# Optimization experiments

Measured on AMD Instinct MI355X. Metric: run time of the kernel, lower is better.

Reference implementation:

```python
import jax, jax.numpy as jnp
import numpy as np

B, N, D, K, S = 16, 1024, 256, 16, 512
TEMP = 0.5   # self.temperature, set externally in the repo
EPS = 1e-10


def _gumbel(key, shape):
    u = jax.random.uniform(key, shape, dtype=jnp.float32)
    return -jnp.log(-jnp.log(u + EPS) + EPS)


def setup_inputs() -> dict:
    key = jax.random.key(0)
    k1, k2, k3 = jax.random.split(key, 3)
    return {
        "ze": jax.random.normal(k1, (B, N, D), dtype=jnp.float32),
        "c_logits": jax.random.normal(k2, (B, K), dtype=jnp.float32),
        "books": jax.random.normal(k3, (K, S, D), dtype=jnp.float32),
        "log_param_q": jnp.asarray(np.log(0.5), dtype=jnp.float32),
        "log_param_q_cls": jnp.asarray(np.log(0.5), dtype=jnp.float32),
        "is_train": 1,
    }


def reference(ze, c_logits, books, log_param_q, log_param_q_cls, is_train):
    # training-path forward of GaussianVectorQuantizer
    param_q = 1.0 + jnp.exp(log_param_q)
    precision_q = 0.5 / jnp.clip(param_q, 1e-10)
    param_q_cls = 1.0 + jnp.exp(log_param_q_cls)
    precision_q_cls = 0.5 / jnp.clip(param_q_cls, 1e-10)

    gkey = jax.random.key(42)
    kg1, kg2 = jax.random.split(gkey)

    # gumbel-softmax over clusters: (B, K)
    c_probs = jax.nn.softmax(
        (c_logits * precision_q_cls + _gumbel(kg1, c_logits.shape)) / TEMP, axis=-1
    )

    # pairwise squared distances to every codebook entry of every cluster: (B, N, K, S)
    z2 = jnp.sum(ze * ze, axis=-1)[:, :, None, None]          # (B, N, 1, 1)
    b2 = jnp.sum(books * books, axis=-1)[None, None]          # (1, 1, K, S)
    cross = jnp.einsum('bnd,ksd->bnks', ze, books)            # (B, N, K, S)
    logit_all = -(z2 - 2.0 * cross + b2) * precision_q        # (B, N, K, S)

    # cluster-probability-weighted logits: (B, N, S)
    logits = jnp.einsum('bnks,bk->bns', logit_all, c_probs)

    # gumbel-softmax encodings per cluster, then weighted codebook matmul
    enc = jax.nn.softmax((logit_all + _gumbel(kg2, logit_all.shape)) / TEMP, axis=-1)
    zq = jnp.einsum('bnks,ksd,bk->bnd', enc, books, c_probs)  # (B, N, D)

    prob = jax.nn.softmax(logits, axis=-1)
    log_prob = jax.nn.log_softmax(logits, axis=-1)
    return zq, precision_q, prob, log_prob
```

## Files before the change

kernel.cpp:

```cpp
#include <hip/hip_runtime.h>
#include <cstdint>
#include <cstddef>

#define JAX_PARTITIONABLE 1

namespace {

constexpr int Bsz = 16, Nn = 1024, Dd = 256, Kk = 16, Ss = 512;
constexpr uint32_t BN = (uint32_t)Bsz * Nn;
constexpr int ZQ_SIZE = Bsz * Nn * Dd;
constexpr int PQ_OFF = ZQ_SIZE;
constexpr int PROB_OFF = ZQ_SIZE + 1;
constexpr int BNS = Bsz * Nn * Ss;
constexpr int LP_OFF = PROB_OFF + BNS;

constexpr int WS_CP = 0;
constexpr int WS_B2 = 256;
constexpr int WS_WB2 = WS_B2 + Kk * Ss;
constexpr int WS_WBF = WS_WB2 + Bsz * Ss;
constexpr int WS_BBF = WS_WBF + Bsz * Ss * Dd;
constexpr int WS_BTF = WS_BBF + (Kk * Ss * Dd) / 2;

constexpr float LOG2E = 1.4426950408889634f;

typedef __attribute__((ext_vector_type(8))) short bf16x8;
typedef __attribute__((ext_vector_type(4))) short short4v;
typedef __attribute__((ext_vector_type(4))) float f32x4;

__device__ __forceinline__ float hw_exp2(float x) { return __builtin_amdgcn_exp2f(x); }
__device__ __forceinline__ float hw_log2(float x) { return __builtin_amdgcn_logf(x); }

struct KP { uint32_t a, b; };

__host__ __device__ constexpr KP tf2x32(uint32_t k0, uint32_t k1,
                                        uint32_t x0, uint32_t x1) {
  uint32_t ks[3] = {k0, k1, k0 ^ k1 ^ 0x1BD11BDAu};
  const int rot[2][4] = {{13, 15, 26, 6}, {17, 29, 16, 24}};
  x0 += ks[0];
  x1 += ks[1];
#pragma unroll
  for (int i = 0; i < 5; ++i) {
#pragma unroll
    for (int j = 0; j < 4; ++j) {
      int r = rot[i & 1][j];
      x0 += x1;
      x1 = (x1 << r) | (x1 >> (32 - r));
      x1 ^= x0;
    }
    x0 += ks[(i + 1) % 3];
    x1 += ks[(i + 2) % 3] + (uint32_t)(i + 1);
  }
  return {x0, x1};
}

#if JAX_PARTITIONABLE
constexpr KP KG1 = tf2x32(0u, 42u, 0u, 0u);
constexpr KP KG2 = tf2x32(0u, 42u, 0u, 1u);
#else
constexpr KP KH0 = tf2x32(0u, 42u, 0u, 2u);
constexpr KP KH1 = tf2x32(0u, 42u, 1u, 3u);
constexpr KP KG1 = {KH0.a, KH1.a};
constexpr KP KG2 = {KH0.b, KH1.b};
#endif

__device__ __forceinline__ float jax_gumbel(KP key, uint32_t idx, uint32_t half) {
#if JAX_PARTITIONABLE
  (void)half;
  KP h = tf2x32(key.a, key.b, 0u, idx);
  uint32_t bits = h.a ^ h.b;
#else
  uint32_t lo = idx < half ? idx : idx - half;
  KP h = tf2x32(key.a, key.b, lo, lo + half);
  uint32_t bits = idx < half ? h.a : h.b;
#endif
  float u = __uint_as_float((bits >> 9) | 0x3F800000u) - 1.0f;
  return -__logf(-__logf(u + 1e-10f) + 1e-10f);
}

__device__ __forceinline__ float jax_gumbel_w2(KP key, uint32_t idx) {
  KP h = tf2x32(key.a, key.b, 0u, idx);
  uint32_t bits = h.a ^ h.b;
  float u = __uint_as_float((bits >> 9) | 0x3F800000u) - 1.0f;
  float y = -__logf(u + 1e-10f) + 1e-10f;
  return -2.0f * hw_log2(y);
}

__device__ __forceinline__ float prec_q(const float* p) {
  return 0.5f / fmaxf(1.0f + expf(p[0]), 1e-10f);
}

__device__ __forceinline__ short f2bf(float x) {
  uint32_t u = __float_as_uint(x);
  uint32_t r = (u + 0x7FFFu + ((u >> 16) & 1u)) >> 16;
  return (short)r;
}

__global__ void __launch_bounds__(256) cprobs_kernel(
    const float* __restrict__ c_logits, const float* __restrict__ lpq,
    const float* __restrict__ lpq_cls, float* __restrict__ ws,
    float* __restrict__ out) {
  __shared__ float sl[256];
  const int t = threadIdx.x;
  const float pqc = prec_q(lpq_cls);
  float g = jax_gumbel(KG1, (uint32_t)t, 128u);
  sl[t] = (c_logits[t] * pqc + g) * 2.0f;
  __syncthreads();
  const int b = t >> 4;
  float m = -3.0e38f;
  for (int j = 0; j < 16; ++j) m = fmaxf(m, sl[b * 16 + j]);
  float sum = 0.f;
  for (int j = 0; j < 16; ++j) sum += expf(sl[b * 16 + j] - m);
  ws[WS_CP + t] = expf(sl[t] - m) / sum;
  if (t == 0) out[PQ_OFF] = prec_q(lpq);
}

__global__ void __launch_bounds__(256) norms_kernel(
    const float* __restrict__ books, float* __restrict__ ws) {
  const int row = blockIdx.x * 4 + (threadIdx.x >> 6);
  const int lane = threadIdx.x & 63;
  float4 v = ((const float4*)(books + (size_t)row * Dd))[lane];
  float s = v.x * v.x + v.y * v.y + v.z * v.z + v.w * v.w;
#pragma unroll
  for (int d = 1; d < 64; d <<= 1) s += __shfl_xor(s, d);
  if (lane == 0) ws[WS_B2 + row] = s;
}

__global__ void __launch_bounds__(256) prep_kernel(
    const float* __restrict__ books, float* __restrict__ ws) {
  __shared__ short tile[16 * 256];
  const int k = blockIdx.x >> 5;
  const int s0 = (blockIdx.x & 31) << 4;
  short* bbf = (short*)(ws + WS_BBF);
  short* btf = (short*)(ws + WS_BTF);
  const int t = threadIdx.x;
#pragma unroll
  for (int i = 0; i < 4; ++i) {
    int idx = t + 256 * i;
    int r = idx >> 6, dq = idx & 63;
    float4 v = ((const float4*)books)[(size_t)(k * Ss + s0 + r) * 64 + dq];
    short4v h = {f2bf(v.x), f2bf(v.y), f2bf(v.z), f2bf(v.w)};
    *(short4v*)&bbf[(size_t)(k * Ss + s0 + r) * 256 + dq * 4] = h;
    *(short4v*)&tile[r * 256 + dq * 4] = h;
  }
  __syncthreads();
  const int d = t;
  short vals[16];
#pragma unroll
  for (int r = 0; r < 16; ++r) vals[r] = tile[r * 256 + d];
  bf16x8 lo, hi;
#pragma unroll
  for (int r = 0; r < 8; ++r) { lo[r] = vals[r]; hi[r] = vals[r + 8]; }
  size_t base = ((size_t)(k * 256 + d)) * 512 + s0;
  *(bf16x8*)&btf[base] = lo;
  *(bf16x8*)&btf[base + 8] = hi;
}

__global__ void __launch_bounds__(256) wbooks_kernel(
    const float* __restrict__ books, float* __restrict__ ws) {
  const int bs = blockIdx.x;
  const int b = bs >> 9, s = bs & 511;
  const int d = threadIdx.x;
  const float* cp = ws + WS_CP + b * 16;
  float acc = 0.f;
#pragma unroll
  for (int k = 0; k < 16; ++k)
    acc = fmaf(cp[k], books[((size_t)(k * Ss + s)) * Dd + d], acc);
  short* wbf = (short*)(ws + WS_WBF);
  wbf[((size_t)(b * Ss + s)) * Dd + d] = f2bf(acc);
  if (d == 0) {
    float a2 = 0.f;
#pragma unroll
    for (int k = 0; k < 16; ++k) a2 = fmaf(cp[k], ws[WS_B2 + k * Ss + s], a2);
    ws[WS_WB2 + b * Ss + s] = a2;
  }
}

__global__ void __launch_bounds__(512, 4) fused_kernel(
    const float* __restrict__ ze, const float* __restrict__ lpq,
    const float* __restrict__ ws, float* __restrict__ out) {
  __shared__ short ze_s[32 * 264];
  __shared__ short enc_s[32 * 520];
  __shared__ float2 redms[32][9];
  __shared__ float cpk[16];

  const int t = threadIdx.x;
  const int w = t >> 6, lane = t & 63, c = lane & 15, q = lane >> 4;
  const float pq = prec_q(lpq);

  if (blockIdx.x < 512) {
    const int b = blockIdx.x >> 5;
    const int n0 = (blockIdx.x & 31) << 5;
    const short* bbf = (const short*)(ws + WS_BBF);
    const short* btf = (const short*)(ws + WS_BTF);
    const float* b2p = ws + WS_B2;
    const float ca = 4.f * pq * LOG2E;
    const float cbs = -2.f * pq * LOG2E;

    if (t < 16) cpk[t] = ws[WS_CP + b * 16 + t];
#pragma unroll
    for (int i = 0; i < 4; ++i) {
      int idx = t + 512 * i;
      int r = idx >> 6, dq = idx & 63;
      float4 v = ((const float4*)ze)[(size_t)(b * Nn + n0 + r) * 64 + dq];
      short4v h = {f2bf(v.x), f2bf(v.y), f2bf(v.z), f2bf(v.w)};
      *(short4v*)&ze_s[r * 264 + dq * 4] = h;
    }
    __syncthreads();

    f32x4 acc2[2][2];
#pragma unroll
    for (int rt = 0; rt < 2; ++rt)
#pragma unroll
      for (int dt = 0; dt < 2; ++dt) acc2[rt][dt] = (f32x4)(0.f);

    for (int k = 0; k < 16; ++k) {
      f32x4 acc1[2][4];
#pragma unroll
      for (int rt = 0; rt < 2; ++rt)
#pragma unroll
        for (int st = 0; st < 4; ++st) acc1[rt][st] = (f32x4)(0.f);
      for (int dstep = 0; dstep < 8; ++dstep) {
        bf16x8 a0 = *(const bf16x8*)&ze_s[(c) * 264 + dstep * 32 + q * 8];
        bf16x8 a1 = *(const bf16x8*)&ze_s[(16 + c) * 264 + dstep * 32 + q * 8];
#pragma unroll
        for (int st = 0; st < 4; ++st) {
          bf16x8 bB = *(const bf16x8*)&bbf[((size_t)(k * Ss + w * 64 + st * 16 + c)) * 256 +
                                           dstep * 32 + q * 8];
          acc1[0][st] = __builtin_amdgcn_mfma_f32_16x16x32_bf16(a0, bB, acc1[0][st], 0, 0, 0);
          acc1[1][st] = __builtin_amdgcn_mfma_f32_16x16x32_bf16(a1, bB, acc1[1][st], 0, 0, 0);
        }
      }

      float cb[4];
#pragma unroll
      for (int st = 0; st < 4; ++st) cb[st] = cbs * b2p[k * Ss + w * 64 + st * 16 + c];
      float mx[2][4], sm[2][4];
#pragma unroll
      for (int rt = 0; rt < 2; ++rt)
#pragma unroll
        for (int reg = 0; reg < 4; ++reg) mx[rt][reg] = -3.0e38f;
#pragma unroll
      for (int rt = 0; rt < 2; ++rt)
#pragma unroll
        for (int st = 0; st < 4; ++st)
#pragma unroll
          for (int reg = 0; reg < 4; ++reg) {
            int row = n0 + rt * 16 + q * 4 + reg;
            uint32_t gi = ((uint32_t)(b * Nn + row) * (uint32_t)Kk + (uint32_t)k) * (uint32_t)Ss +
                          (uint32_t)(w * 64 + st * 16 + c);
            float gw = jax_gumbel_w2(KG2, gi);
            float v = fmaf(acc1[rt][st][reg], ca, cb[st]) + gw;
            acc1[rt][st][reg] = v;
            mx[rt][reg] = fmaxf(mx[rt][reg], v);
          }
#pragma unroll
      for (int m = 1; m < 16; m <<= 1)
#pragma unroll
        for (int rt = 0; rt < 2; ++rt)
#pragma unroll
          for (int reg = 0; reg < 4; ++reg)
            mx[rt][reg] = fmaxf(mx[rt][reg], __shfl_xor(mx[rt][reg], m));
#pragma unroll
      for (int rt = 0; rt < 2; ++rt)
#pragma unroll
        for (int reg = 0; reg < 4; ++reg) sm[rt][reg] = 0.f;
#pragma unroll
      for (int rt = 0; rt < 2; ++rt)
#pragma unroll
        for (int st = 0; st < 4; ++st)
#pragma unroll
          for (int reg = 0; reg < 4; ++reg) {
            float e = hw_exp2(acc1[rt][st][reg] - mx[rt][reg]);
            acc1[rt][st][reg] = e;
            sm[rt][reg] += e;
          }
#pragma unroll
      for (int m = 1; m < 16; m <<= 1)
#pragma unroll
        for (int rt = 0; rt < 2; ++rt)
#pragma unroll
          for (int reg = 0; reg < 4; ++reg) sm[rt][reg] += __shfl_xor(sm[rt][reg], m);
      if (c == 0) {
#pragma unroll
        for (int rt = 0; rt < 2; ++rt)
#pragma unroll
          for (int reg = 0; reg < 4; ++reg) {
            int rl = rt * 16 + q * 4 + reg;
            redms[rl][w] = make_float2(mx[rt][reg], sm[rt][reg]);
          }
      }
      __syncthreads();

      const float cpv = cpk[k];
#pragma unroll
      for (int rt = 0; rt < 2; ++rt)
#pragma unroll
        for (int reg = 0; reg < 4; ++reg) {
          int rl = rt * 16 + q * 4 + reg;
          float M = mx[rt][reg];
#pragma unroll
          for (int w2 = 0; w2 < 8; ++w2) M = fmaxf(M, redms[rl][w2].x);
          float T = 0.f;
#pragma unroll
          for (int w2 = 0; w2 < 8; ++w2)
            T = fmaf(redms[rl][w2].y, hw_exp2(redms[rl][w2].x - M), T);
          float scale = cpv * hw_exp2(mx[rt][reg] - M) * __builtin_amdgcn_rcpf(T);
#pragma unroll
          for (int st = 0; st < 4; ++st)
            enc_s[rl * 520 + w * 64 + st * 16 + c] = f2bf(acc1[rt][st][reg] * scale);
        }
      __syncthreads();

      for (int ss = 0; ss < 16; ++ss) {
        bf16x8 a0 = *(const bf16x8*)&enc_s[(c) * 520 + ss * 32 + q * 8];
        bf16x8 a1 = *(const bf16x8*)&enc_s[(16 + c) * 520 + ss * 32 + q * 8];
#pragma unroll
        for (int dt = 0; dt < 2; ++dt) {
          bf16x8 bB = *(const bf16x8*)&btf[((size_t)(k * 256 + w * 32 + dt * 16 + c)) * 512 +
                                           ss * 32 + q * 8];
          acc2[0][dt] = __builtin_amdgcn_mfma_f32_16x16x32_bf16(a0, bB, acc2[0][dt], 0, 0, 0);
          acc2[1][dt] = __builtin_amdgcn_mfma_f32_16x16x32_bf16(a1, bB, acc2[1][dt], 0, 0, 0);
        }
      }
    }

#pragma unroll
    for (int rt = 0; rt < 2; ++rt)
#pragma unroll
      for (int dt = 0; dt < 2; ++dt)
#pragma unroll
        for (int reg = 0; reg < 4; ++reg) {
          int row = n0 + rt * 16 + q * 4 + reg;
          int d = w * 32 + dt * 16 + c;
          out[(size_t)(b * Nn + row) * Dd + d] = acc2[rt][dt][reg];
        }
  } else {
    const int mbid = blockIdx.x - 512;
    const int b = mbid >> 5;
    const int n0 = (mbid & 31) << 5;
    const short* wbf = (const short*)(ws + WS_WBF);
    const float* wb2 = ws + WS_WB2;

#pragma unroll
    for (int i = 0; i < 4; ++i) {
      int idx = t + 512 * i;
      int r = idx >> 6, dq = idx & 63;
      float4 v = ((const float4*)ze)[(size_t)(b * Nn + n0 + r) * 64 + dq];
      short4v h = {f2bf(v.x), f2bf(v.y), f2bf(v.z), f2bf(v.w)};
      *(short4v*)&ze_s[r * 264 + dq * 4] = h;
    }
    __syncthreads();

    f32x4 acc1[2][4];
#pragma unroll
    for (int rt = 0; rt < 2; ++rt)
#pragma unroll
      for (int st = 0; st < 4; ++st) acc1[rt][st] = (f32x4)(0.f);
    for (int dstep = 0; dstep < 8; ++dstep) {
      bf16x8 a0 = *(const bf16x8*)&ze_s[(c) * 264 + dstep * 32 + q * 8];
      bf16x8 a1 = *(const bf16x8*)&ze_s[(16 + c) * 264 + dstep * 32 + q * 8];
#pragma unroll
      for (int st = 0; st < 4; ++st) {
        bf16x8 bB = *(const bf16x8*)&wbf[((size_t)(b * Ss + w * 64 + st * 16 + c)) * 256 +
                                         dstep * 32 + q * 8];
        acc1[0][st] = __builtin_amdgcn_mfma_f32_16x16x32_bf16(a0, bB, acc1[0][st], 0, 0, 0);
        acc1[1][st] = __builtin_amdgcn_mfma_f32_16x16x32_bf16(a1, bB, acc1[1][st], 0, 0, 0);
      }
    }

    float mx[2][4], sm[2][4];
#pragma unroll
    for (int rt = 0; rt < 2; ++rt)
#pragma unroll
      for (int reg = 0; reg < 4; ++reg) mx[rt][reg] = -3.0e38f;
#pragma unroll
    for (int st = 0; st < 4; ++st) {
      const float wb2v = wb2[b * Ss + w * 64 + st * 16 + c];
#pragma unroll
      for (int rt = 0; rt < 2; ++rt)
#pragma unroll
        for (int reg = 0; reg < 4; ++reg) {
          float v = (2.f * acc1[rt][st][reg] - wb2v) * pq;
          acc1[rt][st][reg] = v;
          mx[rt][reg] = fmaxf(mx[rt][reg], v);
        }
    }
#pragma unroll
    for (int m = 1; m < 16; m <<= 1)
#pragma unroll
      for (int rt = 0; rt < 2; ++rt)
#pragma unroll
        for (int reg = 0; reg < 4; ++reg)
          mx[rt][reg] = fmaxf(mx[rt][reg], __shfl_xor(mx[rt][reg], m));
#pragma unroll
    for (int rt = 0; rt < 2; ++rt)
#pragma unroll
      for (int reg = 0; reg < 4; ++reg) sm[rt][reg] = 0.f;
#pragma unroll
    for (int st = 0; st < 4; ++st)
#pragma unroll
      for (int rt = 0; rt < 2; ++rt)
#pragma unroll
        for (int reg = 0; reg < 4; ++reg)
          sm[rt][reg] += __expf(acc1[rt][st][reg] - mx[rt][reg]);
#pragma unroll
    for (int m = 1; m < 16; m <<= 1)
#pragma unroll
      for (int rt = 0; rt < 2; ++rt)
#pragma unroll
        for (int reg = 0; reg < 4; ++reg) sm[rt][reg] += __shfl_xor(sm[rt][reg], m);
    if (c == 0) {
#pragma unroll
      for (int rt = 0; rt < 2; ++rt)
#pragma unroll
        for (int reg = 0; reg < 4; ++reg)
          redms[rt * 16 + q * 4 + reg][w] = make_float2(mx[rt][reg], sm[rt][reg]);
    }
    __syncthreads();

#pragma unroll
    for (int rt = 0; rt < 2; ++rt)
#pragma unroll
      for (int reg = 0; reg < 4; ++reg) {
        int rl = rt * 16 + q * 4 + reg;
        float M = mx[rt][reg];
#pragma unroll
        for (int w2 = 0; w2 < 8; ++w2) M = fmaxf(M, redms[rl][w2].x);
        float T = 0.f;
#pragma unroll
        for (int w2 = 0; w2 < 8; ++w2)
          T = fmaf(redms[rl][w2].y, __expf(redms[rl][w2].x - M), T);
        const float invT = __builtin_amdgcn_rcpf(T);
        const float lT = __logf(T);
        const size_t base = (size_t)(b * Nn + n0 + rl) * Ss;
#pragma unroll
        for (int st = 0; st < 4; ++st) {
          int s = w * 64 + st * 16 + c;
          float v = acc1[rt][st][reg] - M;
          out[PROB_OFF + base + s] = __expf(v) * invT;
          out[LP_OFF + base + s] = v - lT;
        }
      }
  }
}

}

extern "C" void kernel_launch(void* const* d_in, const int* in_sizes, int n_in,
                              void* d_out, int out_size, void* d_ws, size_t ws_size,
                              hipStream_t stream) {
  (void)in_sizes; (void)n_in; (void)out_size; (void)ws_size;
  const float* ze = (const float*)d_in[0];
  const float* c_logits = (const float*)d_in[1];
  const float* books = (const float*)d_in[2];
  const float* lpq = (const float*)d_in[3];
  const float* lpq_cls = (const float*)d_in[4];
  float* out = (float*)d_out;
  float* ws = (float*)d_ws;

  hipLaunchKernelGGL(cprobs_kernel, dim3(1), dim3(256), 0, stream,
                     c_logits, lpq, lpq_cls, ws, out);
  hipLaunchKernelGGL(norms_kernel, dim3(Kk * Ss / 4), dim3(256), 0, stream, books, ws);
  hipLaunchKernelGGL(prep_kernel, dim3(Kk * 32), dim3(256), 0, stream, books, ws);
  hipLaunchKernelGGL(wbooks_kernel, dim3(Bsz * Ss), dim3(256), 0, stream, books, ws);
  hipLaunchKernelGGL(fused_kernel, dim3(1024), dim3(512), 0, stream,
                     ze, lpq, ws, out);
}
```

Measured before the change: 724.0 us.

## Enlarge fused kernel tile to 64 rows with 16 waves per block

The fused kernel now uses 1024-thread blocks that each handle 64 rows instead of 32. Each wave covers 32 codebook columns and 16 output dims across 4 row tiles. The goal is to halve redundant global reads of the bf16 codebooks per row and raise MFMA reuse of each B fragment. The cross-wave softmax reduction becomes a two-step one: 64 threads compute the final max and inverse sum into shared memory, which adds a barrier. The larger block means more LDS per block and fewer blocks (512) in flight, and __launch_bounds__(1024,4) may force register spills.

```diff
diff --git a/kernel.cpp b/kernel.cpp
--- a/kernel.cpp
+++ b/kernel.cpp
@@ -175,21 +175,26 @@
   }
 }
 
-__global__ void __launch_bounds__(512, 4) fused_kernel(
+__global__ void __launch_bounds__(1024, 4) fused_kernel(
     const float* __restrict__ ze, const float* __restrict__ lpq,
     const float* __restrict__ ws, float* __restrict__ out) {
-  __shared__ short ze_s[32 * 264];
-  __shared__ short enc_s[32 * 520];
-  __shared__ float2 redms[32][9];
+  __shared__ short ze_s[64 * 264];
+  __shared__ short enc_s[64 * 520];
+  __shared__ float redmax[64][17];
+  __shared__ float redsum[64][17];
+  __shared__ float finalM[64];
+  __shared__ float finalI[64];
+  __shared__ float finalL[64];
   __shared__ float cpk[16];
 
   const int t = threadIdx.x;
-  const int w = t >> 6, lane = t & 63, c = lane & 15, q = lane >> 4;
+  const int w = t >> 6;
+  const int lane = t & 63, c = lane & 15, q = lane >> 4;
   const float pq = prec_q(lpq);
 
-  if (blockIdx.x < 512) {
-    const int b = blockIdx.x >> 5;
-    const int n0 = (blockIdx.x & 31) << 5;
+  if (blockIdx.x < 256) {
+    const int b = blockIdx.x >> 4;
+    const int n0 = (blockIdx.x & 15) << 6;
     const short* bbf = (const short*)(ws + WS_BBF);
     const short* btf = (const short*)(ws + WS_BTF);
     const float* b2p = ws + WS_B2;
@@ -199,7 +204,7 @@
     if (t < 16) cpk[t] = ws[WS_CP + b * 16 + t];
 #pragma unroll
     for (int i = 0; i < 4; ++i) {
-      int idx = t + 512 * i;
+      int idx = t + 1024 * i;
       int r = idx >> 6, dq = idx & 63;
       float4 v = ((const float4*)ze)[(size_t)(b * Nn + n0 + r) * 64 + dq];
       short4v h = {f2bf(v.x), f2bf(v.y), f2bf(v.z), f2bf(v.w)};
@@ -207,47 +212,48 @@
     }
     __syncthreads();
 
-    f32x4 acc2[2][2];
-#pragma unroll
-    for (int rt = 0; rt < 2; ++rt)
-#pragma unroll
-      for (int dt = 0; dt < 2; ++dt) acc2[rt][dt] = (f32x4)(0.f);
+    f32x4 acc2[4];
+#pragma unroll
+    for (int rt = 0; rt < 4; ++rt) acc2[rt] = (f32x4)(0.f);
 
     for (int k = 0; k < 16; ++k) {
-      f32x4 acc1[2][4];
-#pragma unroll
-      for (int rt = 0; rt < 2; ++rt)
-#pragma unroll
-        for (int st = 0; st < 4; ++st) acc1[rt][st] = (f32x4)(0.f);
+      f32x4 acc1[4][2];
+#pragma unroll
+      for (int rt = 0; rt < 4; ++rt)
+#pragma unroll
+        for (int st = 0; st < 2; ++st) acc1[rt][st] = (f32x4)(0.f);
       for (int dstep = 0; dstep < 8; ++dstep) {
-        bf16x8 a0 = *(const bf16x8*)&ze_s[(c) * 264 + dstep * 32 + q * 8];
-        bf16x8 a1 = *(const bf16x8*)&ze_s[(16 + c) * 264 + dstep * 32 + q * 8];
-#pragma unroll
-        for (int st = 0; st < 4; ++st) {
-          bf16x8 bB = *(const bf16x8*)&bbf[((size_t)(k * Ss + w * 64 + st * 16 + c)) * 256 +
+        bf16x8 a[4];
+#pragma unroll
+        for (int rt = 0; rt < 4; ++rt)
+          a[rt] = *(const bf16x8*)&ze_s[(rt * 16 + c) * 264 + dstep * 32 + q * 8];
+#pragma unroll
+        for (int st = 0; st < 2; ++st) {
+          bf16x8 bB = *(const bf16x8*)&bbf[((size_t)(k * Ss + w * 32 + st * 16 + c)) * 256 +
                                            dstep * 32 + q * 8];
-          acc1[0][st] = __builtin_amdgcn_mfma_f32_16x16x32_bf16(a0, bB, acc1[0][st], 0, 0, 0);
-          acc1[1][st] = __builtin_amdgcn_mfma_f32_16x16x32_bf16(a1, bB, acc1[1][st], 0, 0, 0);
+#pragma unroll
+          for (int rt = 0; rt < 4; ++rt)
+            acc1[rt][st] = __builtin_amdgcn_mfma_f32_16x16x32_bf16(a[rt], bB, acc1[rt][st], 0, 0, 0);
         }
       }
 
-      float cb[4];
-#pragma unroll
-      for (int st = 0; st < 4; ++st) cb[st] = cbs * b2p[k * Ss + w * 64 + st * 16 + c];
-      float mx[2][4], sm[2][4];
-#pragma unroll
-      for (int rt = 0; rt < 2; ++rt)
+      float cb[2];
+#pragma unroll
+      for (int st = 0; st < 2; ++st) cb[st] = cbs * b2p[k * Ss + w * 32 + st * 16 + c];
+      float mx[4][4], sm[4][4];
+#pragma unroll
+      for (int rt = 0; rt < 4; ++rt)
 #pragma unroll
         for (int reg = 0; reg < 4; ++reg) mx[rt][reg] = -3.0e38f;
 #pragma unroll
-      for (int rt = 0; rt < 2; ++rt)
-#pragma unroll
-        for (int st = 0; st < 4; ++st)
+      for (int rt = 0; rt < 4; ++rt)
+#pragma unroll
+        for (int st = 0; st < 2; ++st)
 #pragma unroll
           for (int reg = 0; reg < 4; ++reg) {
             int row = n0 + rt * 16 + q * 4 + reg;
             uint32_t gi = ((uint32_t)(b * Nn + row) * (uint32_t)Kk + (uint32_t)k) * (uint32_t)Ss +
-                          (uint32_t)(w * 64 + st * 16 + c);
+                          (uint32_t)(w * 32 + st * 16 + c);
             float gw = jax_gumbel_w2(KG2, gi);
             float v = fmaf(acc1[rt][st][reg], ca, cb[st]) + gw;
             acc1[rt][st][reg] = v;
@@ -256,94 +262,100 @@
 #pragma unroll
       for (int m = 1; m < 16; m <<= 1)
 #pragma unroll
-        for (int rt = 0; rt < 2; ++rt)
+        for (int rt = 0; rt < 4; ++rt)
 #pragma unroll
           for (int reg = 0; reg < 4; ++reg)
             mx[rt][reg] = fmaxf(mx[rt][reg], __shfl_xor(mx[rt][reg], m));
-#pragma unroll
-      for (int rt = 0; rt < 2; ++rt)
-#pragma unroll
-        for (int reg = 0; reg < 4; ++reg) sm[rt][reg] = 0.f;
-#pragma unroll
-      for (int rt = 0; rt < 2; ++rt)
-#pragma unroll
-        for (int st = 0; st < 4; ++st)
+      float smv[4][4];
+#pragma unroll
+      for (int rt = 0; rt < 4; ++rt)
+#pragma unroll
+        for (int reg = 0; reg < 4; ++reg) smv[rt][reg] = 0.f;
+#pragma unroll
+      for (int rt = 0; rt < 4; ++rt)
+#pragma unroll
+        for (int st = 0; st < 2; ++st)
 #pragma unroll
           for (int reg = 0; reg < 4; ++reg) {
             float e = hw_exp2(acc1[rt][st][reg] - mx[rt][reg]);
             acc1[rt][st][reg] = e;
-            sm[rt][reg] += e;
+            smv[rt][reg] += e;
           }
 #pragma unroll
       for (int m = 1; m < 16; m <<= 1)
 #pragma unroll
-        for (int rt = 0; rt < 2; ++rt)
-#pragma unroll
-          for (int reg = 0; reg < 4; ++reg) sm[rt][reg] += __shfl_xor(sm[rt][reg], m);
+        for (int rt = 0; rt < 4; ++rt)
+#pragma unroll
+          for (int reg = 0; reg < 4; ++reg) smv[rt][reg] += __shfl_xor(smv[rt][reg], m);
       if (c == 0) {
 #pragma unroll
-        for (int rt = 0; rt < 2; ++rt)
+        for (int rt = 0; rt < 4; ++rt)
 #pragma unroll
           for (int reg = 0; reg < 4; ++reg) {
             int rl = rt * 16 + q * 4 + reg;
-            redms[rl][w] = make_float2(mx[rt][reg], sm[rt][reg]);
+            redmax[rl][w] = mx[rt][reg];
+            redsum[rl][w] = smv[rt][reg];
           }
       }
       __syncthreads();
 
+      if (t < 64) {
+        float M = redmax[t][0];
+#pragma unroll
+        for (int w2 = 1; w2 < 16; ++w2) M = fmaxf(M, redmax[t][w2]);
+        float T = 0.f;
+#pragma unroll
+        for (int w2 = 0; w2 < 16; ++w2)
+          T = fmaf(redsum[t][w2], hw_exp2(redmax[t][w2] - M), T);
+        finalM[t] = M;
+        finalI[t] = __builtin_amdgcn_rcpf(T);
+      }
+      __syncthreads();
+
       const float cpv = cpk[k];
 #pragma unroll
-      for (int rt = 0; rt < 2; ++rt)
+      for (int rt = 0; rt < 4; ++rt)
 #pragma unroll
         for (int reg = 0; reg < 4; ++reg) {
           int rl = rt * 16 + q * 4 + reg;
-          float M = mx[rt][reg];
-#pragma unroll
-          for (int w2 = 0; w2 < 8; ++w2) M = fmaxf(M, redms[rl][w2].x);
-          float T = 0.f;
-#pragma unroll
-          for (int w2 = 0; w2 < 8; ++w2)
-            T = fmaf(redms[rl][w2].y, hw_exp2(redms[rl][w2].x - M), T);
-          float scale = cpv * hw_exp2(mx[rt][reg] - M) * __builtin_amdgcn_rcpf(T);
-#pragma unroll
-          for (int st = 0; st < 4; ++st)
-            enc_s[rl * 520 + w * 64 + st * 16 + c] = f2bf(acc1[rt][st][reg] * scale);
+          float scale = cpv * hw_exp2(mx[rt][reg] - finalM[rl]) * finalI[rl];
+#pragma unroll
+          for (int st = 0; st < 2; ++st)
+            enc_s[rl * 520 + w * 32 + st * 16 + c] = f2bf(acc1[rt][st][reg] * scale);
         }
       __syncthreads();
 
       for (int ss = 0; ss < 16; ++ss) {
-        bf16x8 a0 = *(const bf16x8*)&enc_s[(c) * 520 + ss * 32 + q * 8];
-        bf16x8 a1 = *(const bf16x8*)&enc_s[(16 + c) * 520 + ss * 32 + q * 8];
-#pragma unroll
-        for (int dt = 0; dt < 2; ++dt) {
-          bf16x8 bB = *(const bf16x8*)&btf[((size_t)(k * 256 + w * 32 + dt * 16 + c)) * 512 +
-                                           ss * 32 + q * 8];
-          acc2[0][dt] = __builtin_amdgcn_mfma_f32_16x16x32_bf16(a0, bB, acc2[0][dt], 0, 0, 0);
-          acc2[1][dt] = __builtin_amdgcn_mfma_f32_16x16x32_bf16(a1, bB, acc2[1][dt], 0, 0, 0);
-        }
-      }
-    }
-
-#pragma unroll
-    for (int rt = 0; rt < 2; ++rt)
-#pragma unroll
-      for (int dt = 0; dt < 2; ++dt)
-#pragma unroll
-        for (int reg = 0; reg < 4; ++reg) {
-          int row = n0 + rt * 16 + q * 4 + reg;
-          int d = w * 32 + dt * 16 + c;
-          out[(size_t)(b * Nn + row) * Dd + d] = acc2[rt][dt][reg];
-        }
+        bf16x8 a[4];
+#pragma unroll
+        for (int rt = 0; rt < 4; ++rt)
+          a[rt] = *(const bf16x8*)&enc_s[(rt * 16 + c) * 520 + ss * 32 + q * 8];
+        bf16x8 bB = *(const bf16x8*)&btf[((size_t)(k * 256 + w * 16 + c)) * 512 +
+                                         ss * 32 + q * 8];
+#pragma unroll
+        for (int rt = 0; rt < 4; ++rt)
+          acc2[rt] = __builtin_amdgcn_mfma_f32_16x16x32_bf16(a[rt], bB, acc2[rt], 0, 0, 0);
+      }
+    }
+
+#pragma unroll
+    for (int rt = 0; rt < 4; ++rt)
+#pragma unroll
+      for (int reg = 0; reg < 4; ++reg) {
+        int row = n0 + rt * 16 + q * 4 + reg;
+        int d = w * 16 + c;
+        out[(size_t)(b * Nn + row) * Dd + d] = acc2[rt][reg];
+      }
   } else {
-    const int mbid = blockIdx.x - 512;
-    const int b = mbid >> 5;
-    const int n0 = (mbid & 31) << 5;
+    const int mbid = blockIdx.x - 256;
+    const int b = mbid >> 4;
+    const int n0 = (mbid & 15) << 6;
     const short* wbf = (const short*)(ws + WS_WBF);
     const float* wb2 = ws + WS_WB2;
 
 #pragma unroll
     for (int i = 0; i < 4; ++i) {
-      int idx = t + 512 * i;
+      int idx = t + 1024 * i;
       int r = idx >> 6, dq = idx & 63;
       float4 v = ((const float4*)ze)[(size_t)(b * Nn + n0 + r) * 64 + dq];
       short4v h = {f2bf(v.x), f2bf(v.y), f2bf(v.z), f2bf(v.w)};
@@ -351,33 +363,36 @@
     }
     __syncthreads();
 
-    f32x4 acc1[2][4];
-#pragma unroll
-    for (int rt = 0; rt < 2; ++rt)
-#pragma unroll
-      for (int st = 0; st < 4; ++st) acc1[rt][st] = (f32x4)(0.f);
+    f32x4 acc1[4][2];
+#pragma unroll
+    for (int rt = 0; rt < 4; ++rt)
+#pragma unroll
+      for (int st = 0; st < 2; ++st) acc1[rt][st] = (f32x4)(0.f);
     for (int dstep = 0; dstep < 8; ++dstep) {
-      bf16x8 a0 = *(const bf16x8*)&ze_s[(c) * 264 + dstep * 32 + q * 8];
-      bf16x8 a1 = *(const bf16x8*)&ze_s[(16 + c) * 264 + dstep * 32 + q * 8];
-#pragma unroll
-      for (int st = 0; st < 4; ++st) {
-        bf16x8 bB = *(const bf16x8*)&wbf[((size_t)(b * Ss + w * 64 + st * 16 + c)) * 256 +
+      bf16x8 a[4];
+#pragma unroll
+      for (int rt = 0; rt < 4; ++rt)
+        a[rt] = *(const bf16x8*)&ze_s[(rt * 16 + c) * 264 + dstep * 32 + q * 8];
+#pragma unroll
+      for (int st = 0; st < 2; ++st) {
+        bf16x8 bB = *(const bf16x8*)&wbf[((size_t)(b * Ss + w * 32 + st * 16 + c)) * 256 +
                                          dstep * 32 + q * 8];
-        acc1[0][st] = __builtin_amdgcn_mfma_f32_16x16x32_bf16(a0, bB, acc1[0][st], 0, 0, 0);
-        acc1[1][st] = __builtin_amdgcn_mfma_f32_16x16x32_bf16(a1, bB, acc1[1][st], 0, 0, 0);
-      }
-    }
-
-    float mx[2][4], sm[2][4];
-#pragma unroll
-    for (int rt = 0; rt < 2; ++rt)
+#pragma unroll
+        for (int rt = 0; rt < 4; ++rt)
+          acc1[rt][st] = __builtin_amdgcn_mfma_f32_16x16x32_bf16(a[rt], bB, acc1[rt][st], 0, 0, 0);
+      }
+    }
+
+    float mx[4][4], sm[4][4];
+#pragma unroll
+    for (int rt = 0; rt < 4; ++rt)
 #pragma unroll
       for (int reg = 0; reg < 4; ++reg) mx[rt][reg] = -3.0e38f;
 #pragma unroll
-    for (int st = 0; st < 4; ++st) {
-      const float wb2v = wb2[b * Ss + w * 64 + st * 16 + c];
-#pragma unroll
-      for (int rt = 0; rt < 2; ++rt)
+    for (int st = 0; st < 2; ++st) {
+      const float wb2v = wb2[b * Ss + w * 32 + st * 16 + c];
+#pragma unroll
+      for (int rt = 0; rt < 4; ++rt)
 #pragma unroll
         for (int reg = 0; reg < 4; ++reg) {
           float v = (2.f * acc1[rt][st][reg] - wb2v) * pq;
@@ -388,54 +403,65 @@
 #pragma unroll
     for (int m = 1; m < 16; m <<= 1)
 #pragma unroll
-      for (int rt = 0; rt < 2; ++rt)
+      for (int rt = 0; rt < 4; ++rt)
 #pragma unroll
         for (int reg = 0; reg < 4; ++reg)
           mx[rt][reg] = fmaxf(mx[rt][reg], __shfl_xor(mx[rt][reg], m));
 #pragma unroll
-    for (int rt = 0; rt < 2; ++rt)
+    for (int rt = 0; rt < 4; ++rt)
 #pragma unroll
       for (int reg = 0; reg < 4; ++reg) sm[rt][reg] = 0.f;
 #pragma unroll
-    for (int st = 0; st < 4; ++st)
-#pragma unroll
-      for (int rt = 0; rt < 2; ++rt)
+    for (int st = 0; st < 2; ++st)
+#pragma unroll
+      for (int rt = 0; rt < 4; ++rt)
 #pragma unroll
         for (int reg = 0; reg < 4; ++reg)
           sm[rt][reg] += __expf(acc1[rt][st][reg] - mx[rt][reg]);
 #pragma unroll
     for (int m = 1; m < 16; m <<= 1)
 #pragma unroll
-      for (int rt = 0; rt < 2; ++rt)
+      for (int rt = 0; rt < 4; ++rt)
 #pragma unroll
         for (int reg = 0; reg < 4; ++reg) sm[rt][reg] += __shfl_xor(sm[rt][reg], m);
     if (c == 0) {
 #pragma unroll
-      for (int rt = 0; rt < 2; ++rt)
-#pragma unroll
-        for (int reg = 0; reg < 4; ++reg)
-          redms[rt * 16 + q * 4 + reg][w] = make_float2(mx[rt][reg], sm[rt][reg]);
+      for (int rt = 0; rt < 4; ++rt)
+#pragma unroll
+        for (int reg = 0; reg < 4; ++reg) {
+          int rl = rt * 16 + q * 4 + reg;
+          redmax[rl][w] = mx[rt][reg];
+          redsum[rl][w] = sm[rt][reg];
+        }
     }
     __syncthreads();
 
-#pragma unroll
-    for (int rt = 0; rt < 2; ++rt)
+    if (t < 64) {
+      float M = redmax[t][0];
+#pragma unroll
+      for (int w2 = 1; w2 < 16; ++w2) M = fmaxf(M, redmax[t][w2]);
+      float T = 0.f;
+#pragma unroll
+      for (int w2 = 0; w2 < 16; ++w2)
+        T = fmaf(redsum[t][w2], __expf(redmax[t][w2] - M), T);
+      finalM[t] = M;
+      finalI[t] = __builtin_amdgcn_rcpf(T);
+      finalL[t] = __logf(T);
+    }
+    __syncthreads();
+
+#pragma unroll
+    for (int rt = 0; rt < 4; ++rt)
 #pragma unroll
       for (int reg = 0; reg < 4; ++reg) {
         int rl = rt * 16 + q * 4 + reg;
-        float M = mx[rt][reg];
-#pragma unroll
-        for (int w2 = 0; w2 < 8; ++w2) M = fmaxf(M, redms[rl][w2].x);
-        float T = 0.f;
-#pragma unroll
-        for (int w2 = 0; w2 < 8; ++w2)
-          T = fmaf(redms[rl][w2].y, __expf(redms[rl][w2].x - M), T);
-        const float invT = __builtin_amdgcn_rcpf(T);
-        const float lT = __logf(T);
+        const float M = finalM[rl];
+        const float invT = finalI[rl];
+        const float lT = finalL[rl];
         const size_t base = (size_t)(b * Nn + n0 + rl) * Ss;
 #pragma unroll
-        for (int st = 0; st < 4; ++st) {
-          int s = w * 64 + st * 16 + c;
+        for (int st = 0; st < 2; ++st) {
+          int s = w * 32 + st * 16 + c;
           float v = acc1[rt][st][reg] - M;
           out[PROB_OFF + base + s] = __expf(v) * invT;
           out[LP_OFF + base + s] = v - lT;
@@ -463,6 +489,6 @@
   hipLaunchKernelGGL(norms_kernel, dim3(Kk * Ss / 4), dim3(256), 0, stream, books, ws);
   hipLaunchKernelGGL(prep_kernel, dim3(Kk * 32), dim3(256), 0, stream, books, ws);
   hipLaunchKernelGGL(wbooks_kernel, dim3(Bsz * Ss), dim3(256), 0, stream, books, ws);
-  hipLaunchKernelGGL(fused_kernel, dim3(1024), dim3(512), 0, stream,
+  hipLaunchKernelGGL(fused_kernel, dim3(512), dim3(1024), 0, stream,
                      ze, lpq, ws, out);
 }
```

Result: slower. 744.8 us (+2.9%).
